# Performance work log

Measured on AMD Instinct MI355X. Metric: run time of the kernel, lower is better.

## Reference

```python
import jax, jax.numpy as jnp
import numpy as np

Q, C, T = 256, 128, 128
L = Q + C + T            # 512
D = 1024                 # d_model
H = 8                    # heads
DK = D // H              # 128 = self_attn.d_k
F = 3                    # num_latent_relations
R = 50                   # num_relation_kinds = len(relations2id)
FF = 4 * D               # feed-forward hidden
DEFAULT_QQ_ID = 0        # relations2id['q:q-default']
EPS = 1e-5


def setup_inputs():
    key = jax.random.key(0)
    ks = jax.random.split(key, 40)
    s = 0.02
    def nrm(k, shape, scale=s):
        return jax.random.normal(k, shape, jnp.float32) * scale
    inp = {
        'x': jax.random.normal(ks[0], (1, L, D), jnp.float32),
        'qc_relation': jax.random.uniform(ks[1], (Q, C, F), jnp.float32),
        'cq_relation': jax.random.uniform(ks[2], (C, Q, F), jnp.float32),
        'qt_relation': jax.random.uniform(ks[3], (Q, T, F), jnp.float32),
        'tq_relation': jax.random.uniform(ks[4], (T, Q, F), jnp.float32),
        'ct_relation': jax.random.randint(ks[5], (C + T, C + T), 0, R, jnp.int32),
        'predefined_relation': jax.random.randint(ks[6], (L, L), 0, R, jnp.int32),
        'mask': jnp.ones((1, L, L), jnp.int32),
        # relation embedding tables
        'rel_k_emb': nrm(ks[7], (R, DK)), 'rel_v_emb': nrm(ks[8], (R, DK)),
        'lqc_k': nrm(ks[9], (F, DK)), 'lqc_v': nrm(ks[10], (F, DK)),
        'lcq_k': nrm(ks[11], (F, DK)), 'lcq_v': nrm(ks[12], (F, DK)),
        'lqt_k': nrm(ks[13], (F, DK)), 'lqt_v': nrm(ks[14], (F, DK)),
        'ltq_k': nrm(ks[15], (F, DK)), 'ltq_v': nrm(ks[16], (F, DK)),
        # attention projections (torch Linear: y = x @ W.T + b)
        'Wq': nrm(ks[17], (D, D)), 'bq': jnp.zeros((D,), jnp.float32),
        'Wk': nrm(ks[18], (D, D)), 'bk': jnp.zeros((D,), jnp.float32),
        'Wv': nrm(ks[19], (D, D)), 'bv': jnp.zeros((D,), jnp.float32),
        'Wo': nrm(ks[20], (D, D)), 'bo': jnp.zeros((D,), jnp.float32),
        # layer norms
        'ln1_g': jnp.ones((D,), jnp.float32), 'ln1_b': jnp.zeros((D,), jnp.float32),
        'ln2_g': jnp.ones((D,), jnp.float32), 'ln2_b': jnp.zeros((D,), jnp.float32),
        # FFN
        'W1': nrm(ks[21], (FF, D)), 'b1': jnp.zeros((FF,), jnp.float32),
        'W2': nrm(ks[22], (D, FF)), 'b2': jnp.zeros((D,), jnp.float32),
    }
    return inp


def layer_norm(x, g, b):
    m = jnp.mean(x, -1, keepdims=True)
    v = jnp.mean((x - m) ** 2, -1, keepdims=True)
    return (x - m) * jax.lax.rsqrt(v + EPS) * g + b


def build_latent_relation(ct, qc, cq, qt, tq, emb, lqc, lcq, lqt, ltq):
    # qq block: every entry is the default-qq embedding row
    qq = jnp.broadcast_to(emb[DEFAULT_QQ_ID], (Q, Q, DK))
    qc_e = jnp.einsum('qcf,fd->qcd', qc, lqc)
    cq_e = jnp.einsum('cqf,fd->cqd', cq, lcq)
    qt_e = jnp.einsum('qtf,fd->qtd', qt, lqt)
    tq_e = jnp.einsum('tqf,fd->tqd', tq, ltq)
    ct_e = emb[ct]                                      # [(c+t),(c+t),DK]
    top = jnp.concatenate([qq, qc_e, qt_e], axis=1)      # [Q, L, DK]
    bot = jnp.concatenate([jnp.concatenate([cq_e, tq_e], 0), ct_e], axis=1)  # [C+T, L, DK]
    return jnp.concatenate([top, bot], axis=0)           # [L, L, DK]


def relation_attention(x, rel_k, rel_v, mask, Wq, bq, Wk, bk, Wv, bv, Wo, bo):
    B = x.shape[0]
    def proj(W, b):
        return (x @ W.T + b).reshape(B, L, H, DK).transpose(0, 2, 1, 3)  # [B,H,L,DK]
    q, k, v = proj(Wq, bq), proj(Wk, bk), proj(Wv, bv)
    scores = (jnp.einsum('bhid,bhjd->bhij', q, k)
              + jnp.einsum('bhid,ijd->bhij', q, rel_k)) / jnp.sqrt(jnp.float32(DK))
    scores = jnp.where(mask[:, None] == 0, jnp.float32(-1e9), scores)
    p = jax.nn.softmax(scores, axis=-1)
    o = (jnp.einsum('bhij,bhjd->bhid', p, v)
         + jnp.einsum('bhij,ijd->bhid', p, rel_v))
    o = o.transpose(0, 2, 1, 3).reshape(B, L, D)
    return o @ Wo.T + bo


def reference(x, qc_relation, cq_relation, qt_relation, tq_relation,
              ct_relation, predefined_relation, mask,
              rel_k_emb, rel_v_emb, lqc_k, lqc_v, lcq_k, lcq_v,
              lqt_k, lqt_v, ltq_k, ltq_v,
              Wq, bq, Wk, bk, Wv, bv, Wo, bo,
              ln1_g, ln1_b, ln2_g, ln2_b, W1, b1, W2, b2):
    # latent relation build + combine with predefined lookup
    rel_k = (rel_k_emb[predefined_relation]
             + build_latent_relation(ct_relation, qc_relation, cq_relation,
                                     qt_relation, tq_relation,
                                     rel_k_emb, lqc_k, lcq_k, lqt_k, ltq_k))
    rel_v = (rel_v_emb[predefined_relation]
             + build_latent_relation(ct_relation, qc_relation, cq_relation,
                                     qt_relation, tq_relation,
                                     rel_v_emb, lqc_v, lcq_v, lqt_v, ltq_v))
    # sublayer 0: pre-norm relation-biased self attention (dropout=0)
    h = x + relation_attention(layer_norm(x, ln1_g, ln1_b), rel_k, rel_v, mask,
                               Wq, bq, Wk, bk, Wv, bv, Wo, bo)
    # sublayer 1: pre-norm FFN
    y = layer_norm(h, ln2_g, ln2_b)
    ffn = jax.nn.relu(y @ W1.T + b1) @ W2.T + b2
    return h + ffn
```

## Files before the change

### kernel.cpp

```cpp
#include <hip/hip_runtime.h>
#include <hip/hip_bf16.h>

#define LL 512
#define DD 1024
#define HH 8
#define DKK 128
#define QQ 256
#define CCC 128
#define TTT 128
#define RR 50
#define FFF 4096
#define KLD 576
#define SLD 576

typedef __attribute__((ext_vector_type(8))) short short8;
typedef __attribute__((ext_vector_type(4))) float float4v;

__device__ __forceinline__ unsigned short f2bu(float f) {
  __hip_bfloat16 h = __float2bfloat16(f);
  unsigned short u; __builtin_memcpy(&u, &h, 2); return u;
}
__device__ __forceinline__ float b2f(unsigned short u) {
  unsigned int v = ((unsigned int)u) << 16;
  float f; __builtin_memcpy(&f, &v, 4); return f;
}
__device__ __forceinline__ int4 cvt8(float4 x, float4 y) {
  int4 o;
  o.x = (int)f2bu(x.x) | ((int)f2bu(x.y) << 16);
  o.y = (int)f2bu(x.z) | ((int)f2bu(x.w) << 16);
  o.z = (int)f2bu(y.x) | ((int)f2bu(y.y) << 16);
  o.w = (int)f2bu(y.z) | ((int)f2bu(y.w) << 16);
  return o;
}

__device__ __forceinline__ void lds_barrier() {
  __builtin_amdgcn_sched_barrier(0);
  __builtin_amdgcn_s_waitcnt(0xC07F);
  __builtin_amdgcn_s_barrier();
  __builtin_amdgcn_sched_barrier(0);
}

#define LOADSET(A0,A1,B0,B1,F0,F1,F2,F3,itv) { int k0v = (itv) << 6;          \
  A0 = *(const int4*)(Az + (size_t)(bm + r)*lda + k0v + gc*8);                \
  A1 = *(const int4*)(Az + (size_t)(bm + 32 + r)*lda + k0v + gc*8);           \
  if constexpr (!CONVB) {                                                     \
    B0 = *(const int4*)(Bz16 + (size_t)(bnb + r)*ldb + k0v + gc*8);           \
    if constexpr (NB > 1)                                                     \
      B1 = *(const int4*)(Bz16 + (size_t)(bnb + 32 + r)*ldb + k0v + gc*8);    \
  } else {                                                                    \
    F0 = *(const float4*)(Bz32 + (size_t)(bnb + r)*ldb + k0v + gc*8);         \
    F1 = *(const float4*)(Bz32 + (size_t)(bnb + r)*ldb + k0v + gc*8 + 4);     \
    if constexpr (NB > 1) {                                                   \
      F2 = *(const float4*)(Bz32 + (size_t)(bnb + 32 + r)*ldb + k0v + gc*8);  \
      F3 = *(const float4*)(Bz32 + (size_t)(bnb + 32 + r)*ldb + k0v + gc*8 + 4); } } }

#define STORESET2(basep,A0,A1,B0,B1,F0,F1,F2,F3) {                            \
  char* bse = (basep);                                                        \
  *(int4*)(bse + r*128 + sl*16) = A0;                                         \
  *(int4*)(bse + (32 + r)*128 + sl*16) = A1;                                  \
  if constexpr (!CONVB) {                                                     \
    *(int4*)(bse + ABYTES + r*128 + sl*16) = B0;                              \
    if constexpr (NB > 1)                                                     \
      *(int4*)(bse + ABYTES + (32 + r)*128 + sl*16) = B1;                     \
  } else {                                                                    \
    *(int4*)(bse + ABYTES + r*128 + sl*16) = cvt8(F0, F1);                    \
    if constexpr (NB > 1)                                                     \
      *(int4*)(bse + ABYTES + (32 + r)*128 + sl*16) = cvt8(F2, F3); } }


__global__ __launch_bounds__(256) void kprep_kernel(
    const float* __restrict__ embk,
    const float* __restrict__ lqc, const float* __restrict__ lqt,
    const float* __restrict__ lcq, const float* __restrict__ ltq,
    unsigned short* __restrict__ Kh)
{
  int g = blockIdx.x*256 + threadIdx.x;
  if (g >= 8*64*128) return;
  int d = g & 127, rr = (g >> 7) & 63, h = g >> 13;
  float v = 0.f;
  if (rr < 50) v = embk[rr*128 + d];
  else if (rr < 62) {
    int u = rr - 50; int tb = u/3, f = u - tb*3;
    const float* tab = (tb==0) ? lqc : (tb==1) ? lqt : (tb==2) ? lcq : ltq;
    v = tab[f*128 + d];
  }
  Kh[(((size_t)h*16 + (d>>3))*KLD + 512 + rr)*8 + (d&7)] = f2bu(v);
}

__global__ __launch_bounds__(256) void ln_bf16_kernel(const float* __restrict__ x,
    const float* __restrict__ g, const float* __restrict__ b,
    unsigned short* __restrict__ y)
{
  int row = blockIdx.x, t = threadIdx.x;
  const float4 xv = ((const float4*)(x + row*DD))[t];
  float s  = xv.x+xv.y+xv.z+xv.w;
  float ss = xv.x*xv.x+xv.y*xv.y+xv.z*xv.z+xv.w*xv.w;
  __shared__ float rs[256], rss[256];
  rs[t]=s; rss[t]=ss; __syncthreads();
  for (int st=128; st>0; st>>=1){ if (t<st){ rs[t]+=rs[t+st]; rss[t]+=rss[t+st]; } __syncthreads(); }
  float mean = rs[0] * (1.0f/DD);
  float var  = rss[0]*(1.0f/DD) - mean*mean;
  float inv  = rsqrtf(var + 1e-5f);
  float4 gv = ((const float4*)g)[t], bv = ((const float4*)b)[t];
  ushort4 ov;
  ov.x = f2bu((xv.x-mean)*inv*gv.x + bv.x);
  ov.y = f2bu((xv.y-mean)*inv*gv.y + bv.y);
  ov.z = f2bu((xv.z-mean)*inv*gv.z + bv.z);
  ov.w = f2bu((xv.w-mean)*inv*gv.w + bv.w);
  ((ushort4*)(y + row*DD))[t] = ov;
}

__global__ __launch_bounds__(256) void ln_bf16_addb_kernel(float* __restrict__ x,
    const float* __restrict__ g, const float* __restrict__ b,
    const float* __restrict__ b2, unsigned short* __restrict__ y)
{
  int row = blockIdx.x, t = threadIdx.x;
  const float4 xv = ((const float4*)(x + row*DD))[t];
  float s  = xv.x+xv.y+xv.z+xv.w;
  float ss = xv.x*xv.x+xv.y*xv.y+xv.z*xv.z+xv.w*xv.w;
  __shared__ float rs[256], rss[256];
  rs[t]=s; rss[t]=ss; __syncthreads();
  for (int st=128; st>0; st>>=1){ if (t<st){ rs[t]+=rs[t+st]; rss[t]+=rss[t+st]; } __syncthreads(); }
  float mean = rs[0] * (1.0f/DD);
  float var  = rss[0]*(1.0f/DD) - mean*mean;
  float inv  = rsqrtf(var + 1e-5f);
  float4 gv = ((const float4*)g)[t], bv = ((const float4*)b)[t];
  ushort4 ov;
  ov.x = f2bu((xv.x-mean)*inv*gv.x + bv.x);
  ov.y = f2bu((xv.y-mean)*inv*gv.y + bv.y);
  ov.z = f2bu((xv.z-mean)*inv*gv.z + bv.z);
  ov.w = f2bu((xv.w-mean)*inv*gv.w + bv.w);
  ((ushort4*)(y + row*DD))[t] = ov;
  float4 b2v = ((const float4*)b2)[t];
  float4 nx; nx.x = xv.x+b2v.x; nx.y = xv.y+b2v.y; nx.z = xv.z+b2v.z; nx.w = xv.w+b2v.w;
  ((float4*)(x + row*DD))[t] = nx;
}

template<int BN, int DEPTH, int CONVB, int ZK, int OUT_BF16, int RELU, int HAS_SRC, int HAS_BIAS>
__global__ __launch_bounds__(256) void gemm_pl(
    const unsigned short* __restrict__ A, int lda, size_t sAz,
    const void* __restrict__ Bv, int ldb, size_t sBz,
    const float* __restrict__ bias,
    const float* __restrict__ src, int ldsrc, size_t sSz,
    void* __restrict__ Cv, int ldc, size_t sCz,
    int K)
{
  constexpr int BM = 64;
  constexpr int WM = 32, WN = BN/2, FM = 2, FN = WN/16;
  constexpr int NB = BN/32;
  constexpr int ABYTES = BM*128, TILE = ABYTES + BN*128;
  __shared__ char lds[2*TILE];
  int t = threadIdx.x, w = t >> 6, l = t & 63;
  size_t z = blockIdx.z;
  const unsigned short* Az = A + z*sAz;
  const unsigned short* Bz16 = (const unsigned short*)Bv + (CONVB ? 0 : z*sBz);
  const float*          Bz32 = (const float*)Bv + (CONVB ? z*sBz : 0);
  int bm = blockIdx.y*BM, bn = blockIdx.x*BN;
  int bnb = bn;
  int wm = (w>>1)*WM, wn = (w&1)*WN;

  float4v acc[FM][FN];
  #pragma unroll
  for (int m=0;m<FM;++m)
    #pragma unroll
    for (int n=0;n<FN;++n) acc[m][n] = (float4v){0.f,0.f,0.f,0.f};

  int r = t >> 3, sl = t & 7;
  int gc = sl ^ (r & 7);
  int quad = l >> 4, lrow = l & 15;
  const int nit = K >> 6;

  int4 Aa0, Aa1, Ab0, Ab1;  float4 Af0, Af1, Af2, Af3;
  int4 Ba0, Ba1, Bb0, Bb1;  float4 Bf0, Bf1, Bf2, Bf3;
  int4 Ca0, Ca1, Cb0, Cb1;  float4 Cf0, Cf1, Cf2, Cf3;
  int4 Da0, Da1, Db0, Db1;  float4 Df0, Df1, Df2, Df3;

  auto compute = [&](const char* base) {
    const char* ab = base;
    const char* bb = base + ABYTES;
    #pragma unroll
    for (int step=0; step<2; ++step) {
      int c = step*4 + quad;
      short8 af[FM], bf[FN];
      #pragma unroll
      for (int m=0;m<FM;++m) {
        int Rw = wm + m*16 + lrow;
        af[m] = *(const short8*)(ab + Rw*128 + ((c ^ (Rw & 7))*16));
      }
      #pragma unroll
      for (int n=0;n<FN;++n) {
        int Rw = wn + n*16 + lrow;
        bf[n] = *(const short8*)(bb + Rw*128 + ((c ^ (Rw & 7))*16));
      }
      #pragma unroll
      for (int m=0;m<FM;++m)
        #pragma unroll
        for (int n=0;n<FN;++n)
          acc[m][n] = __builtin_amdgcn_mfma_f32_16x16x32_bf16(af[m], bf[n], acc[m][n], 0, 0, 0);
    }
  };

  if constexpr (DEPTH == 2) {
    LOADSET(Aa0,Aa1,Ab0,Ab1,Af0,Af1,Af2,Af3, 0);
    LOADSET(Ba0,Ba1,Bb0,Bb1,Bf0,Bf1,Bf2,Bf3, 1);
    for (int it = 0; it < nit; it += 2) {
      STORESET2(lds, Aa0,Aa1,Ab0,Ab1,Af0,Af1,Af2,Af3);
      if (it + 2 < nit) LOADSET(Aa0,Aa1,Ab0,Ab1,Af0,Af1,Af2,Af3, it+2);
      lds_barrier();
      compute(lds);
      STORESET2(lds + TILE, Ba0,Ba1,Bb0,Bb1,Bf0,Bf1,Bf2,Bf3);
      if (it + 3 < nit) LOADSET(Ba0,Ba1,Bb0,Bb1,Bf0,Bf1,Bf2,Bf3, it+3);
      lds_barrier();
      compute(lds + TILE);
    }
  } else {
    LOADSET(Aa0,Aa1,Ab0,Ab1,Af0,Af1,Af2,Af3, 0);
    LOADSET(Ba0,Ba1,Bb0,Bb1,Bf0,Bf1,Bf2,Bf3, 1);
    LOADSET(Ca0,Ca1,Cb0,Cb1,Cf0,Cf1,Cf2,Cf3, 2);
    LOADSET(Da0,Da1,Db0,Db1,Df0,Df1,Df2,Df3, 3);
    for (int it = 0; it < nit; it += 4) {
      STORESET2(lds, Aa0,Aa1,Ab0,Ab1,Af0,Af1,Af2,Af3);
      if (it + 4 < nit) LOADSET(Aa0,Aa1,Ab0,Ab1,Af0,Af1,Af2,Af3, it+4);
      lds_barrier();
      compute(lds);
      STORESET2(lds + TILE, Ba0,Ba1,Bb0,Bb1,Bf0,Bf1,Bf2,Bf3);
      if (it + 5 < nit) LOADSET(Ba0,Ba1,Bb0,Bb1,Bf0,Bf1,Bf2,Bf3, it+5);
      lds_barrier();
      compute(lds + TILE);
      STORESET2(lds, Ca0,Ca1,Cb0,Cb1,Cf0,Cf1,Cf2,Cf3);
      if (it + 6 < nit) LOADSET(Ca0,Ca1,Cb0,Cb1,Cf0,Cf1,Cf2,Cf3, it+6);
      lds_barrier();
      compute(lds);
      STORESET2(lds + TILE, Da0,Da1,Db0,Db1,Df0,Df1,Df2,Df3);
      if (it + 7 < nit) LOADSET(Da0,Da1,Db0,Db1,Df0,Df1,Df2,Df3, it+7);
      lds_barrier();
      compute(lds + TILE);
    }
  }

  #pragma unroll
  for (int m=0;m<FM;++m)
    #pragma unroll
    for (int n=0;n<FN;++n)
      #pragma unroll
      for (int rg=0;rg<4;++rg) {
        int row = bm + wm + m*16 + quad*4 + rg;
        int col = bn + wn + n*16 + lrow;
        float vv = acc[m][n][rg];
        if (ZK) {
          atomicAdd(&((float*)Cv)[(size_t)row*ldc + col], vv);
        } else {
          if (HAS_BIAS) vv += bias[col];
          if (HAS_SRC)  vv += src[z*sSz + (size_t)row*ldsrc + col];
          if (RELU) vv = fmaxf(vv, 0.f);
          if (OUT_BF16) ((unsigned short*)Cv)[z*sCz + (size_t)row*ldc + col] = f2bu(vv);
          else          ((float*)Cv)[z*sCz + (size_t)row*ldc + col] = vv;
        }
      }
}

__global__ __launch_bounds__(256) void gemm_qkv_pl(
    const unsigned short* __restrict__ A,
    const float* __restrict__ Wq, const float* __restrict__ Wk,
    const float* __restrict__ Wv,
    const float* __restrict__ bq, const float* __restrict__ bk,
    const float* __restrict__ bv,
    unsigned short* __restrict__ Qh, unsigned short* __restrict__ Kh,
    unsigned short* __restrict__ Vt)
{
  constexpr int BN = 64, CONVB = 1;
  constexpr int WM = 32, WN = 32, FM = 2, FN = 2;
  constexpr int NB = 2;
  constexpr int ABYTES = 64*128, TILE = ABYTES + BN*128;
  __shared__ char lds[2*TILE];
  int t = threadIdx.x, w = t >> 6, l = t & 63;
  int bm = blockIdx.y*64, bn = blockIdx.x*BN;
  int wm = (w>>1)*WM, wn = (w&1)*WN;
  const int lda = DD, ldb = DD, nit = DD >> 6;
  const unsigned short* Az = A;
  int part0 = bn >> 10;
  const float* Bz32 = (part0==0 ? Wq : part0==1 ? Wk : Wv) + (size_t)(bn & 1023)*DD;
  const unsigned short* Bz16 = nullptr; (void)Bz16;
  int bnb = 0;

  float4v acc[FM][FN];
  #pragma unroll
  for (int m=0;m<FM;++m)
    #pragma unroll
    for (int n=0;n<FN;++n) acc[m][n] = (float4v){0.f,0.f,0.f,0.f};

  int r = t >> 3, sl = t & 7;
  int gc = sl ^ (r & 7);
  int quad = l >> 4, lrow = l & 15;

  int4 Aa0, Aa1, Ab0, Ab1;  float4 Af0, Af1, Af2, Af3;
  int4 Ba0, Ba1, Bb0, Bb1;  float4 Bf0, Bf1, Bf2, Bf3;
  int4 Ca0, Ca1, Cb0, Cb1;  float4 Cf0, Cf1, Cf2, Cf3;
  int4 Da0, Da1, Db0, Db1;  float4 Df0, Df1, Df2, Df3;

  auto compute = [&](const char* base) {
    const char* ab = base;
    const char* bb = base + ABYTES;
    #pragma unroll
    for (int step=0; step<2; ++step) {
      int c = step*4 + quad;
      short8 af[FM], bf[FN];
      #pragma unroll
      for (int m=0;m<FM;++m) {
        int Rw = wm + m*16 + lrow;
        af[m] = *(const short8*)(ab + Rw*128 + ((c ^ (Rw & 7))*16));
      }
      #pragma unroll
      for (int n=0;n<FN;++n) {
        int Rw = wn + n*16 + lrow;
        bf[n] = *(const short8*)(bb + Rw*128 + ((c ^ (Rw & 7))*16));
      }
      #pragma unroll
      for (int m=0;m<FM;++m)
        #pragma unroll
        for (int n=0;n<FN;++n)
          acc[m][n] = __builtin_amdgcn_mfma_f32_16x16x32_bf16(af[m], bf[n], acc[m][n], 0, 0, 0);
    }
  };

  LOADSET(Aa0,Aa1,Ab0,Ab1,Af0,Af1,Af2,Af3, 0);
  LOADSET(Ba0,Ba1,Bb0,Bb1,Bf0,Bf1,Bf2,Bf3, 1);
  LOADSET(Ca0,Ca1,Cb0,Cb1,Cf0,Cf1,Cf2,Cf3, 2);
  LOADSET(Da0,Da1,Db0,Db1,Df0,Df1,Df2,Df3, 3);
  for (int it = 0; it < nit; it += 4) {
    STORESET2(lds, Aa0,Aa1,Ab0,Ab1,Af0,Af1,Af2,Af3);
    if (it + 4 < nit) LOADSET(Aa0,Aa1,Ab0,Ab1,Af0,Af1,Af2,Af3, it+4);
    lds_barrier();
    compute(lds);
    STORESET2(lds + TILE, Ba0,Ba1,Bb0,Bb1,Bf0,Bf1,Bf2,Bf3);
    if (it + 5 < nit) LOADSET(Ba0,Ba1,Bb0,Bb1,Bf0,Bf1,Bf2,Bf3, it+5);
    lds_barrier();
    compute(lds + TILE);
    STORESET2(lds, Ca0,Ca1,Cb0,Cb1,Cf0,Cf1,Cf2,Cf3);
    if (it + 6 < nit) LOADSET(Ca0,Ca1,Cb0,Cb1,Cf0,Cf1,Cf2,Cf3, it+6);
    lds_barrier();
    compute(lds);
    STORESET2(lds + TILE, Da0,Da1,Db0,Db1,Df0,Df1,Df2,Df3);
    if (it + 7 < nit) LOADSET(Da0,Da1,Db0,Db1,Df0,Df1,Df2,Df3, it+7);
    lds_barrier();
    compute(lds + TILE);
  }

  #pragma unroll
  for (int m=0;m<FM;++m)
    #pragma unroll
    for (int n=0;n<FN;++n)
      #pragma unroll
      for (int rg=0;rg<4;++rg) {
        int row = bm + wm + m*16 + quad*4 + rg;
        int col = bn + wn + n*16 + lrow;
        int part = col >> 10, hh = (col >> 7) & 7, d = col & 127;
        const float* bp = (part==0) ? bq : (part==1) ? bk : bv;
        float vv = acc[m][n][rg] + bp[col & 1023];
        unsigned short o = f2bu(vv);
        if (part == 0)      Qh[((size_t)hh*LL + row)*DKK + d] = o;
        else if (part == 1) Kh[(((size_t)hh*16 + (d>>3))*KLD + row)*8 + (d&7)] = o;
        else                Vt[(((size_t)hh*64 + (row>>3))*128 + d)*8 + (row&7)] = o;
      }
}

#define A3_QROWB 272
#define A3_PROWB 1040
#define A3_SROWD 584
#define A3_O2ROW 132
#define A3_OFF_P   2176
#define A3_OFF_S   10496
#define A3_OFF_PW  29184
#define A3_OFF_PF1 30848
#define A3_OFF_PF2 30976
#define A3_OFF_SI  31104
#define A3_OFF_O2  31136
#define A3_LDS     35360

__global__ __launch_bounds__(256) void attn_fused(
    const unsigned short* __restrict__ Qh, const unsigned short* __restrict__ Kh,
    const unsigned short* __restrict__ Vt,
    const float* __restrict__ qcr, const float* __restrict__ cqr,
    const float* __restrict__ qtr, const float* __restrict__ tqr,
    const int* __restrict__ ct, const int* __restrict__ pred,
    const int* __restrict__ mask,
    const float* __restrict__ embv, const float* __restrict__ lqc_v,
    const float* __restrict__ lcq_v, const float* __restrict__ lqt_v,
    const float* __restrict__ ltq_v,
    unsigned short* __restrict__ obuf)
{
  __shared__ __align__(16) char lds[A3_LDS];
  const int t = threadIdx.x;
  const int w = t >> 6, l = t & 63, quad = l >> 4, lrow = l & 15;
  const int i0 = blockIdx.x * 8, h = blockIdx.y;

  for (int k2 = t; k2 < 488; k2 += 256) ((float*)(lds + A3_OFF_PW))[k2] = 0.f;

  if (t < 128) {
    int qr = t >> 4, qc = t & 15;
    *(int4*)(lds + qr*A3_QROWB + qc*16) =
        *(const int4*)(Qh + ((size_t)h*LL + i0 + qr)*DKK + qc*8);
  }
  lds_barrier();

  {
    const unsigned short* Kc = Kh + (size_t)h*16*KLD*8;
    short8 af0 = *(const short8*)(lds + lrow*A3_QROWB + (quad     )*16);
    short8 af1 = *(const short8*)(lds + lrow*A3_QROWB + (quad +  4)*16);
    short8 af2 = *(const short8*)(lds + lrow*A3_QROWB + (quad +  8)*16);
    short8 af3 = *(const short8*)(lds + lrow*A3_QROWB + (quad + 12)*16);
    #pragma unroll
    for (int jt = 0; jt < 9; ++jt) {
      float4v acc = (float4v){0.f,0.f,0.f,0.f};
      int krow = jt*64 + w*16 + lrow;
      short8 bf0 = *(const short8*)(Kc + ((size_t)(quad     )*KLD + krow)*8);
      short8 bf1 = *(const short8*)(Kc + ((size_t)(quad +  4)*KLD + krow)*8);
      short8 bf2 = *(const short8*)(Kc + ((size_t)(quad +  8)*KLD + krow)*8);
      short8 bf3 = *(const short8*)(Kc + ((size_t)(quad + 12)*KLD + krow)*8);
      acc = __builtin_amdgcn_mfma_f32_16x16x32_bf16(af0, bf0, acc, 0, 0, 0);
      acc = __builtin_amdgcn_mfma_f32_16x16x32_bf16(af1, bf1, acc, 0, 0, 0);
      acc = __builtin_amdgcn_mfma_f32_16x16x32_bf16(af2, bf2, acc, 0, 0, 0);
      acc = __builtin_amdgcn_mfma_f32_16x16x32_bf16(af3, bf3, acc, 0, 0, 0);
      if (quad < 2) {
        #pragma unroll
        for (int rg = 0; rg < 4; ++rg)
          ((float*)(lds + A3_OFF_S))[(quad*4 + rg)*A3_SROWD + jt*64 + w*16 + lrow] = acc[rg];
      }
    }
  }
  lds_barrier();

  const int row = t >> 5, l32 = t & 31;
  const int i = i0 + row;
  const float* Sp = (const float*)(lds + A3_OFF_S) + row*A3_SROWD;
  const int bse = (i0 < QQ) ? 562 : (i0 < QQ + CCC) ? 568 : 571;
  const float lq1a = Sp[bse], lq1b = Sp[bse+1], lq1c = Sp[bse+2];
  const float lq2a = Sp[565], lq2b = Sp[566], lq2c = Sp[567];

  float sum=0.f, f0=0.f, f1=0.f, f2=0.f, g0=0.f, g1=0.f, g2=0.f;
  float* pwsrow = (float*)(lds + A3_OFF_PW) + row*52;
  #pragma unroll
  for (int m = 0; m < 16; ++m) {
    int j = m*32 + l32;
    int predv = pred[i*LL + j];
    int maskv = mask[i*LL + j];
    float s = Sp[j] + Sp[512 + predv];
    float c0=0.f, c1=0.f, c2=0.f; int rt; int scat2 = 0;
    if (i0 < QQ) {
      if (j < QQ) { s += Sp[512]; rt = 0; }
      else if (j < QQ + CCC) {
        const float* r3 = qcr + ((size_t)i*CCC + (j - QQ))*3;
        c0 = r3[0]; c1 = r3[1]; c2 = r3[2];
        s += c0*lq1a + c1*lq1b + c2*lq1c; rt = 1;
      } else {
        const float* r3 = qtr + ((size_t)i*TTT + (j - QQ - CCC))*3;
        c0 = r3[0]; c1 = r3[1]; c2 = r3[2];
        s += c0*lq2a + c1*lq2b + c2*lq2c; rt = 2;
      }
    } else {
      if (j < QQ) {
        const float* r3 = (i < QQ + CCC) ? cqr + ((size_t)(i - QQ)*QQ + j)*3
                                         : tqr + ((size_t)(i - QQ - CCC)*QQ + j)*3;
        c0 = r3[0]; c1 = r3[1]; c2 = r3[2];
        s += c0*lq1a + c1*lq1b + c2*lq1c; rt = 1;
      } else {
        scat2 = ct[(i - QQ)*(CCC + TTT) + (j - QQ)];
        s += Sp[512 + scat2]; rt = 0;
      }
    }
    s *= 0.08838834764831845f;
    float e = (maskv == 0) ? 0.f : __expf(s);
    sum += e;
    *(unsigned short*)(lds + A3_OFF_P + row*A3_PROWB + j*2) = f2bu(e);
    atomicAdd(pwsrow + predv, e);
    if (rt == 0)      atomicAdd(pwsrow + scat2, e);
    else if (rt == 1) { f0 += e*c0; f1 += e*c1; f2 += e*c2; }
    else              { g0 += e*c0; g1 += e*c1; g2 += e*c2; }
  }
  #pragma unroll
  for (int off = 16; off >= 1; off >>= 1) {
    sum += __shfl_xor(sum, off);
    f0 += __shfl_xor(f0, off); f1 += __shfl_xor(f1, off); f2 += __shfl_xor(f2, off);
    g0 += __shfl_xor(g0, off); g1 += __shfl_xor(g1, off); g2 += __shfl_xor(g2, off);
  }
  if (l32 == 0) {
    float* pf1 = (float*)(lds + A3_OFF_PF1) + row*4;
    float* pf2 = (float*)(lds + A3_OFF_PF2) + row*4;
    pf1[0] = f0; pf1[1] = f1; pf1[2] = f2;
    pf2[0] = g0; pf2[1] = g1; pf2[2] = g2;
    ((float*)(lds + A3_OFF_SI))[row] = 1.0f / sum;
  }
  lds_barrier();

  {
    int orow = t >> 5, d0 = (t & 31)*4;
    const float* pwsr = (const float*)(lds + A3_OFF_PW) + orow*52;
    float a0=0.f, a1=0.f, a2=0.f, a3=0.f;
    #pragma unroll 5
    for (int rr = 0; rr < RR; ++rr) {
      float pv = pwsr[rr];
      float4 ev = *(const float4*)(embv + rr*DKK + d0);
      a0 += pv*ev.x; a1 += pv*ev.y; a2 += pv*ev.z; a3 += pv*ev.w;
    }
    const float* tab1 = (i0 < QQ) ? lqc_v : (i0 < QQ + CCC) ? lcq_v : ltq_v;
    const float* pf1 = (const float*)(lds + A3_OFF_PF1) + orow*4;
    float4 t0 = *(const float4*)(tab1 + d0);
    float4 t1 = *(const float4*)(tab1 + DKK + d0);
    float4 t2 = *(const float4*)(tab1 + 2*DKK + d0);
    a0 += pf1[0]*t0.x + pf1[1]*t1.x + pf1[2]*t2.x;
    a1 += pf1[0]*t0.y + pf1[1]*t1.y + pf1[2]*t2.y;
    a2 += pf1[0]*t0.z + pf1[1]*t1.z + pf1[2]*t2.z;
    a3 += pf1[0]*t0.w + pf1[1]*t1.w + pf1[2]*t2.w;
    if (i0 < QQ) {
      const float* pf2 = (const float*)(lds + A3_OFF_PF2) + orow*4;
      float4 u0 = *(const float4*)(lqt_v + d0);
      float4 u1 = *(const float4*)(lqt_v + DKK + d0);
      float4 u2 = *(const float4*)(lqt_v + 2*DKK + d0);
      a0 += pf2[0]*u0.x + pf2[1]*u1.x + pf2[2]*u2.x;
      a1 += pf2[0]*u0.y + pf2[1]*u1.y + pf2[2]*u2.y;
      a2 += pf2[0]*u0.z + pf2[1]*u1.z + pf2[2]*u2.z;
      a3 += pf2[0]*u0.w + pf2[1]*u1.w + pf2[2]*u2.w;
    }
    float4 av; av.x=a0; av.y=a1; av.z=a2; av.w=a3;
    *(float4*)((float*)(lds + A3_OFF_O2) + orow*A3_O2ROW + d0) = av;
  }
  lds_barrier();

  float4v oacc0 = (float4v){0.f,0.f,0.f,0.f};
  float4v oacc1 = (float4v){0.f,0.f,0.f,0.f};
  {
    const unsigned short* Vc = Vt + (size_t)h*64*128*8;
    #pragma unroll
    for (int it = 0; it < 8; ++it) {
      #pragma unroll
      for (int kk = 0; kk < 2; ++kk) {
        int c = kk*4 + quad;
        short8 pa  = *(const short8*)(lds + A3_OFF_P + lrow*A3_PROWB + it*128 + c*16);
        short8 vf0 = *(const short8*)(Vc + (((size_t)(it*8 + c))*128 + w*32 + lrow)*8);
        short8 vf1 = *(const short8*)(Vc + (((size_t)(it*8 + c))*128 + w*32 + 16 + lrow)*8);
        oacc0 = __builtin_amdgcn_mfma_f32_16x16x32_bf16(pa, vf0, oacc0, 0, 0, 0);
        oacc1 = __builtin_amdgcn_mfma_f32_16x16x32_bf16(pa, vf1, oacc1, 0, 0, 0);
      }
    }
  }

  if (quad < 2) {
    const float* o2s = (const float*)(lds + A3_OFF_O2);
    const float* sinv = (const float*)(lds + A3_OFF_SI);
    #pragma unroll
    for (int n = 0; n < 2; ++n) {
      int d = w*32 + n*16 + lrow;
      #pragma unroll
      for (int rg = 0; rg < 4; ++rg) {
        int rw = quad*4 + rg;
        float oval = (n==0) ? oacc0[rg] : oacc1[rg];
        float val = (oval + o2s[rw*A3_O2ROW + d]) * sinv[rw];
        obuf[(size_t)(i0 + rw)*DD + h*DKK + d] = f2bu(val);
      }
    }
  }
}

extern "C" void kernel_launch(void* const* d_in, const int* in_sizes, int n_in,
                              void* d_out, int out_size, void* d_ws, size_t ws_size,
                              hipStream_t stream)
{
  const float* x    = (const float*)d_in[0];
  const float* qcr  = (const float*)d_in[1];
  const float* cqr  = (const float*)d_in[2];
  const float* qtr  = (const float*)d_in[3];
  const float* tqr  = (const float*)d_in[4];
  const int*   ct   = (const int*)d_in[5];
  const int*   pred = (const int*)d_in[6];
  const int*   mask = (const int*)d_in[7];
  const float* embk = (const float*)d_in[8];
  const float* embv = (const float*)d_in[9];
  const float* lqc_k = (const float*)d_in[10];
  const float* lqc_v = (const float*)d_in[11];
  const float* lcq_k = (const float*)d_in[12];
  const float* lcq_v = (const float*)d_in[13];
  const float* lqt_k = (const float*)d_in[14];
  const float* lqt_v = (const float*)d_in[15];
  const float* ltq_k = (const float*)d_in[16];
  const float* ltq_v = (const float*)d_in[17];
  const float* Wq = (const float*)d_in[18]; const float* bq = (const float*)d_in[19];
  const float* Wk = (const float*)d_in[20]; const float* bk = (const float*)d_in[21];
  const float* Wv = (const float*)d_in[22]; const float* bv = (const float*)d_in[23];
  const float* Wo = (const float*)d_in[24]; const float* bo = (const float*)d_in[25];
  const float* ln1_g = (const float*)d_in[26]; const float* ln1_b = (const float*)d_in[27];
  const float* ln2_g = (const float*)d_in[28]; const float* ln2_b = (const float*)d_in[29];
  const float* W1 = (const float*)d_in[30]; const float* b1 = (const float*)d_in[31];
  const float* W2 = (const float*)d_in[32]; const float* b2 = (const float*)d_in[33];
  float* out = (float*)d_out;

  float* wsf = (float*)d_ws;
  float* S    = wsf;
  float* o2   = S + (size_t)HH*LL*SLD;
  unsigned short* ub = (unsigned short*)(o2 + (size_t)HH*LL*DKK);
  unsigned short* ybuf_b = ub;
  unsigned short* obuf_b = ybuf_b + LL*DD;
  unsigned short* Qh     = obuf_b + LL*DD;
  unsigned short* Kh     = Qh + (size_t)HH*LL*DKK;
  unsigned short* Vt     = Kh + (size_t)HH*KLD*DKK;
  unsigned short* hidden = (unsigned short*)S;

  kprep_kernel<<<(8*64*128 + 255)/256, 256, 0, stream>>>(
      embk, lqc_k, lqt_k, lcq_k, ltq_k, Kh);
  ln_bf16_kernel<<<LL, 256, 0, stream>>>(x, ln1_g, ln1_b, ybuf_b);
  gemm_qkv_pl<<<dim3(48, 8), 256, 0, stream>>>(ybuf_b, Wq, Wk, Wv, bq, bk, bv,
                                               Qh, Kh, Vt);
  attn_fused<<<dim3(64, 8), 256, 0, stream>>>(
      Qh, Kh, Vt, qcr, cqr, qtr, tqr, ct, pred, mask,
      embv, lqc_v, lcq_v, lqt_v, ltq_v, obuf_b);
  gemm_pl<32,4,1,0,0,0,1,1><<<dim3(32, 8, 1), 256, 0, stream>>>(
      obuf_b, DD, 0, Wo, DD, 0, bo, x, DD, 0, out, DD, 0, DD);
  ln_bf16_addb_kernel<<<LL, 256, 0, stream>>>(out, ln2_g, ln2_b, b2, ybuf_b);
  gemm_pl<64,4,1,0,1,1,0,1><<<dim3(64, 8, 1), 256, 0, stream>>>(
      ybuf_b, DD, 0, W1, DD, 0, b1, nullptr, 0, 0, hidden, FFF, 0, DD);
  gemm_pl<64,4,1,1,0,0,0,0><<<dim3(16, 8, 4), 256, 0, stream>>>(
      hidden, FFF, (size_t)1024, W2, FFF, (size_t)1024,
      nullptr, nullptr, 0, 0, out, DD, 0, 1024);
}
```

Baseline: 235.9 us.

## Use 128x64 GEMM tiles with 512-thread blocks and fold kprep into LayerNorm

The QKV, FFN1 and FFN2 GEMMs move to 128-row by 64-column tiles run by 512 threads (8 waves) per block. Each thread now loads one B row segment instead of two, and each B tile in LDS is reused across twice as many A rows. The separate kprep kernel is merged into the first LayerNorm kernel to save a launch. The trade-off is half as many blocks per grid, which lowers parallelism on a GPU with many CUs, plus larger LDS use per block.

```diff
diff --git a/kernel.cpp b/kernel.cpp
--- a/kernel.cpp
+++ b/kernel.cpp
@@ -67,29 +67,32 @@
     if constexpr (NB > 1)                                                     \
       *(int4*)(bse + ABYTES + (32 + r)*128 + sl*16) = cvt8(F2, F3); } }
 
-
-__global__ __launch_bounds__(256) void kprep_kernel(
+#define LOADSET8(A0,A1,B0,F0,F1,itv) { int k0v = (itv) << 6;                  \
+  A0 = *(const int4*)(Az + (size_t)(bm + r)*lda + k0v + gc*8);                \
+  A1 = *(const int4*)(Az + (size_t)(bm + 64 + r)*lda + k0v + gc*8);           \
+  if constexpr (!CONVB) {                                                     \
+    B0 = *(const int4*)(Bz16 + (size_t)(bnb + r)*ldb + k0v + gc*8);           \
+  } else {                                                                    \
+    F0 = *(const float4*)(Bz32 + (size_t)(bnb + r)*ldb + k0v + gc*8);         \
+    F1 = *(const float4*)(Bz32 + (size_t)(bnb + r)*ldb + k0v + gc*8 + 4); } }
+
+#define STORESET8(basep,A0,A1,B0,F0,F1) {                                     \
+  char* bse = (basep);                                                        \
+  *(int4*)(bse + r*128 + sl*16) = A0;                                         \
+  *(int4*)(bse + (64 + r)*128 + sl*16) = A1;                                  \
+  if constexpr (!CONVB) {                                                     \
+    *(int4*)(bse + ABYTES + r*128 + sl*16) = B0;                              \
+  } else {                                                                    \
+    *(int4*)(bse + ABYTES + r*128 + sl*16) = cvt8(F0, F1); } }
+
+
+__global__ __launch_bounds__(256) void ln_bf16_kernel(const float* __restrict__ x,
+    const float* __restrict__ g, const float* __restrict__ b,
+    unsigned short* __restrict__ y,
     const float* __restrict__ embk,
     const float* __restrict__ lqc, const float* __restrict__ lqt,
     const float* __restrict__ lcq, const float* __restrict__ ltq,
     unsigned short* __restrict__ Kh)
-{
-  int g = blockIdx.x*256 + threadIdx.x;
-  if (g >= 8*64*128) return;
-  int d = g & 127, rr = (g >> 7) & 63, h = g >> 13;
-  float v = 0.f;
-  if (rr < 50) v = embk[rr*128 + d];
-  else if (rr < 62) {
-    int u = rr - 50; int tb = u/3, f = u - tb*3;
-    const float* tab = (tb==0) ? lqc : (tb==1) ? lqt : (tb==2) ? lcq : ltq;
-    v = tab[f*128 + d];
-  }
-  Kh[(((size_t)h*16 + (d>>3))*KLD + 512 + rr)*8 + (d&7)] = f2bu(v);
-}
-
-__global__ __launch_bounds__(256) void ln_bf16_kernel(const float* __restrict__ x,
-    const float* __restrict__ g, const float* __restrict__ b,
-    unsigned short* __restrict__ y)
 {
   int row = blockIdx.x, t = threadIdx.x;
   const float4 xv = ((const float4*)(x + row*DD))[t];
@@ -108,6 +111,18 @@
   ov.z = f2bu((xv.z-mean)*inv*gv.z + bv.z);
   ov.w = f2bu((xv.w-mean)*inv*gv.w + bv.w);
   ((ushort4*)(y + row*DD))[t] = ov;
+  int gg = blockIdx.x*256 + t;
+  if (gg < 8*64*128) {
+    int d = gg & 127, rr = (gg >> 7) & 63, hh = gg >> 13;
+    float v = 0.f;
+    if (rr < 50) v = embk[rr*128 + d];
+    else if (rr < 62) {
+      int u = rr - 50; int tb = u/3, f = u - tb*3;
+      const float* tab = (tb==0) ? lqc : (tb==1) ? lqt : (tb==2) ? lcq : ltq;
+      v = tab[f*128 + d];
+    }
+    Kh[(((size_t)hh*16 + (d>>3))*KLD + 512 + rr)*8 + (d&7)] = f2bu(v);
+  }
 }
 
 __global__ __launch_bounds__(256) void ln_bf16_addb_kernel(float* __restrict__ x,
@@ -259,7 +274,114 @@
       }
 }
 
-__global__ __launch_bounds__(256) void gemm_qkv_pl(
+template<int BN, int CONVB, int ZK, int OUT_BF16, int RELU, int HAS_SRC, int HAS_BIAS>
+__global__ __launch_bounds__(512) void gemm_pl8(
+    const unsigned short* __restrict__ A, int lda, size_t sAz,
+    const void* __restrict__ Bv, int ldb, size_t sBz,
+    const float* __restrict__ bias,
+    const float* __restrict__ src, int ldsrc, size_t sSz,
+    void* __restrict__ Cv, int ldc, size_t sCz,
+    int K)
+{
+  constexpr int BM = 128;
+  constexpr int FM = 2, FN = 2;
+  constexpr int ABYTES = BM*128, TILE = ABYTES + BN*128;
+  __shared__ char lds[2*TILE];
+  int t = threadIdx.x, w = t >> 6, l = t & 63;
+  size_t z = blockIdx.z;
+  const unsigned short* Az = A + z*sAz;
+  const unsigned short* Bz16 = (const unsigned short*)Bv + (CONVB ? 0 : z*sBz);
+  const float*          Bz32 = (const float*)Bv + (CONVB ? z*sBz : 0);
+  int bm = blockIdx.y*BM, bn = blockIdx.x*BN;
+  int bnb = bn;
+  int wm = (w>>1)*32, wn = (w&1)*32;
+
+  float4v acc[FM][FN];
+  #pragma unroll
+  for (int m=0;m<FM;++m)
+    #pragma unroll
+    for (int n=0;n<FN;++n) acc[m][n] = (float4v){0.f,0.f,0.f,0.f};
+
+  int r = t >> 3, sl = t & 7;
+  int gc = sl ^ (r & 7);
+  int quad = l >> 4, lrow = l & 15;
+  const int nit = K >> 6;
+
+  int4 Aa0, Aa1, Ab0;  float4 Af0, Af1;
+  int4 Ba0, Ba1, Bb0;  float4 Bf0, Bf1;
+  int4 Ca0, Ca1, Cb0;  float4 Cf0, Cf1;
+  int4 Da0, Da1, Db0;  float4 Df0, Df1;
+
+  auto compute = [&](const char* base) {
+    const char* ab = base;
+    const char* bb = base + ABYTES;
+    #pragma unroll
+    for (int step=0; step<2; ++step) {
+      int c = step*4 + quad;
+      short8 af[FM], bf[FN];
+      #pragma unroll
+      for (int m=0;m<FM;++m) {
+        int Rw = wm + m*16 + lrow;
+        af[m] = *(const short8*)(ab + Rw*128 + ((c ^ (Rw & 7))*16));
+      }
+      #pragma unroll
+      for (int n=0;n<FN;++n) {
+        int Rw = wn + n*16 + lrow;
+        bf[n] = *(const short8*)(bb + Rw*128 + ((c ^ (Rw & 7))*16));
+      }
+      #pragma unroll
+      for (int m=0;m<FM;++m)
+        #pragma unroll
+        for (int n=0;n<FN;++n)
+          acc[m][n] = __builtin_amdgcn_mfma_f32_16x16x32_bf16(af[m], bf[n], acc[m][n], 0, 0, 0);
+    }
+  };
+
+  LOADSET8(Aa0,Aa1,Ab0,Af0,Af1, 0);
+  LOADSET8(Ba0,Ba1,Bb0,Bf0,Bf1, 1);
+  LOADSET8(Ca0,Ca1,Cb0,Cf0,Cf1, 2);
+  LOADSET8(Da0,Da1,Db0,Df0,Df1, 3);
+  for (int it = 0; it < nit; it += 4) {
+    STORESET8(lds, Aa0,Aa1,Ab0,Af0,Af1);
+    if (it + 4 < nit) LOADSET8(Aa0,Aa1,Ab0,Af0,Af1, it+4);
+    lds_barrier();
+    compute(lds);
+    STORESET8(lds + TILE, Ba0,Ba1,Bb0,Bf0,Bf1);
+    if (it + 5 < nit) LOADSET8(Ba0,Ba1,Bb0,Bf0,Bf1, it+5);
+    lds_barrier();
+    compute(lds + TILE);
+    STORESET8(lds, Ca0,Ca1,Cb0,Cf0,Cf1);
+    if (it + 6 < nit) LOADSET8(Ca0,Ca1,Cb0,Cf0,Cf1, it+6);
+    lds_barrier();
+    compute(lds);
+    STORESET8(lds + TILE, Da0,Da1,Db0,Df0,Df1);
+    if (it + 7 < nit) LOADSET8(Da0,Da1,Db0,Df0,Df1, it+7);
+    lds_barrier();
+    compute(lds + TILE);
+  }
+
+  #pragma unroll
+  for (int m=0;m<FM;++m)
+    #pragma unroll
+    for (int n=0;n<FN;++n)
+      #pragma unroll
+      for (int rg=0;rg<4;++rg) {
+        int row = bm + wm + m*16 + quad*4 + rg;
+        int col = bn + wn + n*16 + lrow;
+        float vv = acc[m][n][rg];
+        if (ZK) {
+          atomicAdd(&((float*)Cv)[(size_t)row*ldc + col], vv);
+        } else {
+          if (HAS_BIAS) vv += bias[col];
+          if (HAS_SRC)  vv += src[z*sSz + (size_t)row*ldsrc + col];
+          if (RELU) vv = fmaxf(vv, 0.f);
+          if (OUT_BF16) ((unsigned short*)Cv)[z*sCz + (size_t)row*ldc + col] = f2bu(vv);
+          else          ((float*)Cv)[z*sCz + (size_t)row*ldc + col] = vv;
+        }
+      }
+}
+
+__global__ __launch_bounds__(512) void gemm_qkv_pl8(
     const unsigned short* __restrict__ A,
     const float* __restrict__ Wq, const float* __restrict__ Wk,
     const float* __restrict__ Wv,
@@ -269,13 +391,12 @@
     unsigned short* __restrict__ Vt)
 {
   constexpr int BN = 64, CONVB = 1;
-  constexpr int WM = 32, WN = 32, FM = 2, FN = 2;
-  constexpr int NB = 2;
-  constexpr int ABYTES = 64*128, TILE = ABYTES + BN*128;
+  constexpr int FM = 2, FN = 2;
+  constexpr int ABYTES = 128*128, TILE = ABYTES + BN*128;
   __shared__ char lds[2*TILE];
   int t = threadIdx.x, w = t >> 6, l = t & 63;
-  int bm = blockIdx.y*64, bn = blockIdx.x*BN;
-  int wm = (w>>1)*WM, wn = (w&1)*WN;
+  int bm = blockIdx.y*128, bn = blockIdx.x*BN;
+  int wm = (w>>1)*32, wn = (w&1)*32;
   const int lda = DD, ldb = DD, nit = DD >> 6;
   const unsigned short* Az = A;
   int part0 = bn >> 10;
@@ -293,10 +414,10 @@
   int gc = sl ^ (r & 7);
   int quad = l >> 4, lrow = l & 15;
 
-  int4 Aa0, Aa1, Ab0, Ab1;  float4 Af0, Af1, Af2, Af3;
-  int4 Ba0, Ba1, Bb0, Bb1;  float4 Bf0, Bf1, Bf2, Bf3;
-  int4 Ca0, Ca1, Cb0, Cb1;  float4 Cf0, Cf1, Cf2, Cf3;
-  int4 Da0, Da1, Db0, Db1;  float4 Df0, Df1, Df2, Df3;
+  int4 Aa0, Aa1, Ab0;  float4 Af0, Af1;
+  int4 Ba0, Ba1, Bb0;  float4 Bf0, Bf1;
+  int4 Ca0, Ca1, Cb0;  float4 Cf0, Cf1;
+  int4 Da0, Da1, Db0;  float4 Df0, Df1;
 
   auto compute = [&](const char* base) {
     const char* ab = base;
@@ -323,25 +444,25 @@
     }
   };
 
-  LOADSET(Aa0,Aa1,Ab0,Ab1,Af0,Af1,Af2,Af3, 0);
-  LOADSET(Ba0,Ba1,Bb0,Bb1,Bf0,Bf1,Bf2,Bf3, 1);
-  LOADSET(Ca0,Ca1,Cb0,Cb1,Cf0,Cf1,Cf2,Cf3, 2);
-  LOADSET(Da0,Da1,Db0,Db1,Df0,Df1,Df2,Df3, 3);
+  LOADSET8(Aa0,Aa1,Ab0,Af0,Af1, 0);
+  LOADSET8(Ba0,Ba1,Bb0,Bf0,Bf1, 1);
+  LOADSET8(Ca0,Ca1,Cb0,Cf0,Cf1, 2);
+  LOADSET8(Da0,Da1,Db0,Df0,Df1, 3);
   for (int it = 0; it < nit; it += 4) {
-    STORESET2(lds, Aa0,Aa1,Ab0,Ab1,Af0,Af1,Af2,Af3);
-    if (it + 4 < nit) LOADSET(Aa0,Aa1,Ab0,Ab1,Af0,Af1,Af2,Af3, it+4);
+    STORESET8(lds, Aa0,Aa1,Ab0,Af0,Af1);
+    if (it + 4 < nit) LOADSET8(Aa0,Aa1,Ab0,Af0,Af1, it+4);
     lds_barrier();
     compute(lds);
-    STORESET2(lds + TILE, Ba0,Ba1,Bb0,Bb1,Bf0,Bf1,Bf2,Bf3);
-    if (it + 5 < nit) LOADSET(Ba0,Ba1,Bb0,Bb1,Bf0,Bf1,Bf2,Bf3, it+5);
+    STORESET8(lds + TILE, Ba0,Ba1,Bb0,Bf0,Bf1);
+    if (it + 5 < nit) LOADSET8(Ba0,Ba1,Bb0,Bf0,Bf1, it+5);
     lds_barrier();
     compute(lds + TILE);
-    STORESET2(lds, Ca0,Ca1,Cb0,Cb1,Cf0,Cf1,Cf2,Cf3);
-    if (it + 6 < nit) LOADSET(Ca0,Ca1,Cb0,Cb1,Cf0,Cf1,Cf2,Cf3, it+6);
+    STORESET8(lds, Ca0,Ca1,Cb0,Cf0,Cf1);
+    if (it + 6 < nit) LOADSET8(Ca0,Ca1,Cb0,Cf0,Cf1, it+6);
     lds_barrier();
     compute(lds);
-    STORESET2(lds + TILE, Da0,Da1,Db0,Db1,Df0,Df1,Df2,Df3);
-    if (it + 7 < nit) LOADSET(Da0,Da1,Db0,Db1,Df0,Df1,Df2,Df3, it+7);
+    STORESET8(lds + TILE, Da0,Da1,Db0,Df0,Df1);
+    if (it + 7 < nit) LOADSET8(Da0,Da1,Db0,Df0,Df1, it+7);
     lds_barrier();
     compute(lds + TILE);
   }
@@ -604,20 +725,19 @@
   unsigned short* Vt     = Kh + (size_t)HH*KLD*DKK;
   unsigned short* hidden = (unsigned short*)S;
 
-  kprep_kernel<<<(8*64*128 + 255)/256, 256, 0, stream>>>(
-      embk, lqc_k, lqt_k, lcq_k, ltq_k, Kh);
-  ln_bf16_kernel<<<LL, 256, 0, stream>>>(x, ln1_g, ln1_b, ybuf_b);
-  gemm_qkv_pl<<<dim3(48, 8), 256, 0, stream>>>(ybuf_b, Wq, Wk, Wv, bq, bk, bv,
-                                               Qh, Kh, Vt);
+  ln_bf16_kernel<<<LL, 256, 0, stream>>>(x, ln1_g, ln1_b, ybuf_b,
+                                         embk, lqc_k, lqt_k, lcq_k, ltq_k, Kh);
+  gemm_qkv_pl8<<<dim3(48, 4), 512, 0, stream>>>(ybuf_b, Wq, Wk, Wv, bq, bk, bv,
+                                                Qh, Kh, Vt);
   attn_fused<<<dim3(64, 8), 256, 0, stream>>>(
       Qh, Kh, Vt, qcr, cqr, qtr, tqr, ct, pred, mask,
       embv, lqc_v, lcq_v, lqt_v, ltq_v, obuf_b);
   gemm_pl<32,4,1,0,0,0,1,1><<<dim3(32, 8, 1), 256, 0, stream>>>(
       obuf_b, DD, 0, Wo, DD, 0, bo, x, DD, 0, out, DD, 0, DD);
   ln_bf16_addb_kernel<<<LL, 256, 0, stream>>>(out, ln2_g, ln2_b, b2, ybuf_b);
-  gemm_pl<64,4,1,0,1,1,0,1><<<dim3(64, 8, 1), 256, 0, stream>>>(
+  gemm_pl8<64,1,0,1,1,0,1><<<dim3(64, 4), 512, 0, stream>>>(
       ybuf_b, DD, 0, W1, DD, 0, b1, nullptr, 0, 0, hidden, FFF, 0, DD);
-  gemm_pl<64,4,1,1,0,0,0,0><<<dim3(16, 8, 4), 256, 0, stream>>>(
+  gemm_pl8<64,1,1,0,0,0,0><<<dim3(16, 4, 4), 512, 0, stream>>>(
       hidden, FFF, (size_t)1024, W2, FFF, (size_t)1024,
       nullptr, nullptr, 0, 0, out, DD, 0, 1024);
 }
```

Result: faster. 229.5 us (median of 2 runs) (-2.7%).
